# Kernel optimization log

Hardware: AMD Instinct MI355X
Metric: run time of the kernel (lower is better)

Reference implementation:

```python
import jax, jax.numpy as jnp
import numpy as np

NUM_PTS = 8   # num_points_per_face
K = 5         # self.k


def _sq_dist(x, y):
    # squared euclidean distance matrix (Nx, Ny); matches torch.cdist**2 / sum((a-b)**2)
    x2 = jnp.sum(x * x, axis=1)[:, None]
    y2 = jnp.sum(y * y, axis=1)[None, :]
    d = x2 + y2 - 2.0 * (x @ y.T)
    return jnp.maximum(d, 0.0)


def setup_inputs() -> dict:
    key = jax.random.key(0)
    k1, k2, k3, k4, k5, k6, k7 = jax.random.split(key, 7)
    V, Fs, Ft = 2048, 4096, 4096
    return {
        "source_vertices": jax.random.normal(k1, (1, V, 3), dtype=jnp.float32),
        "source_faces": jax.random.randint(k2, (Fs, 3), 0, V),
        "target_vertices": jax.random.normal(k3, (1, V, 3), dtype=jnp.float32),
        "target_faces": jax.random.randint(k4, (3, Ft), 0, V),
        "face_probs": jax.random.uniform(k5, (Fs,), dtype=jnp.float32),
        "r1u": jax.random.uniform(k6, (Fs, NUM_PTS), dtype=jnp.float32),
        "r2u": jax.random.uniform(k7, (Fs, NUM_PTS), dtype=jnp.float32),
    }


def reference(source_vertices, source_faces, target_vertices, target_faces, face_probs, r1u, r2u):
    sv = source_vertices[0]                 # (V, 3)
    tv = target_vertices[0]                 # (V, 3)
    tf = target_faces.T                     # (Ft, 3)
    Fs = source_faces.shape[0]

    src_bc = sv[source_faces].mean(axis=1)  # (Fs, 3) source barycenters
    tgt_bc = tv[tf].mean(axis=1)            # (Ft, 3) target barycenters

    # ---- forward loss: prob-weighted min squared distance to target barycenters
    d_fwd = _sq_dist(src_bc, tgt_bc)        # (Fs, Ft)
    forward_loss = jnp.sum(face_probs * jnp.min(d_fwd, axis=1))

    # ---- sample points from triangles via barycentric coords
    r1 = jnp.sqrt(r1u)
    w1 = 1.0 - r1
    w2 = r1 * (1.0 - r2u)
    w3 = r1 * r2u
    v1 = sv[source_faces[:, 0]]             # (Fs, 3)
    v2 = sv[source_faces[:, 1]]
    v3 = sv[source_faces[:, 2]]
    pts = (w1[..., None] * v1[:, None] + w2[..., None] * v2[:, None]
           + w3[..., None] * v3[:, None]).reshape(-1, 3)   # (P, 3), P = Fs*NUM_PTS
    pt_faces = jnp.repeat(jnp.arange(Fs), NUM_PTS)          # (P,)
    pt_probs = face_probs[pt_faces]                         # (P,)

    # ---- reverse loss, batched over all P points
    d_src = _sq_dist(pts, src_bc)                           # (P, Fs)
    neg_d, idx = jax.lax.top_k(-d_src, K + 1)               # K+1 smallest distances
    tri_dists = -neg_d                                      # (P, K+1)
    mask = idx != pt_faces[:, None]                         # exclude own face
    has_self = jnp.any(~mask, axis=1)
    excl_pos = jnp.where(has_self, jnp.argmin(mask, axis=1), K + 1)  # (P,)
    t = jnp.arange(K)
    sel = t[None, :] + (t[None, :] >= excl_pos[:, None]).astype(jnp.int32)  # (P, K)
    valid_dists = jnp.take_along_axis(tri_dists, sel, axis=1)   # (P, K)
    valid_idx = jnp.take_along_axis(idx, sel, axis=1)           # (P, K)
    valid_probs = face_probs[valid_idx]                         # (P, K)

    min_tgt = jnp.min(_sq_dist(pts, tgt_bc), axis=1)            # (P,)

    reverse_loss = jnp.sum(pt_probs * min_tgt
                           + (1.0 - pt_probs) * jnp.mean(valid_probs * valid_dists, axis=1))
    return forward_loss + reverse_loss
```

## Files before the change

kernel.cpp:

```cpp
#include <hip/hip_runtime.h>
#include <math.h>

#define FS 4096
#define FT 4096
#define TS 1024
#define BIGF 3.0e38f
#define KEYINF 0xFFFFFFFFu

__device__ __forceinline__ unsigned umin32(unsigned a, unsigned b) { return a < b ? a : b; }
__device__ __forceinline__ unsigned umax32(unsigned a, unsigned b) { return a < b ? b : a; }

__device__ __forceinline__ unsigned med3u(unsigned a, unsigned b, unsigned c) {
    unsigned d;
    asm("v_med3_u32 %0, %1, %2, %3" : "=v"(d) : "v"(a), "v"(b), "v"(c));
    return d;
}

__device__ __forceinline__ float block_reduce_sum(float v) {
    __shared__ float s[8];
    for (int o = 32; o > 0; o >>= 1) v += __shfl_down(v, o, 64);
    int lane = threadIdx.x & 63, wid = threadIdx.x >> 6;
    if (lane == 0) s[wid] = v;
    __syncthreads();
    int nw = blockDim.x >> 6;
    v = (threadIdx.x < (unsigned)nw) ? s[threadIdx.x] : 0.f;
    if (wid == 0)
        for (int o = 4; o > 0; o >>= 1) v += __shfl_down(v, o, 64);
    return v;
}

#define CE(x, y) { unsigned _n = umin32(x, y); y = umax32(x, y); x = _n; }

__device__ __forceinline__ void merge32(unsigned s[6]) {
    #pragma unroll
    for (int m = 1; m <= 16; m <<= 1) {
        unsigned b0 = __shfl_xor(s[0], m, 64), b1 = __shfl_xor(s[1], m, 64);
        unsigned b2 = __shfl_xor(s[2], m, 64), b3 = __shfl_xor(s[3], m, 64);
        unsigned b4 = __shfl_xor(s[4], m, 64), b5 = __shfl_xor(s[5], m, 64);
        unsigned l0 = s[0], l1 = s[1];
        unsigned l2 = umin32(s[2], b5), l3 = umin32(s[3], b4);
        unsigned l4 = umin32(s[4], b3), l5 = umin32(s[5], b2);
        unsigned l6 = b1, l7 = b0;
        CE(l0, l4) CE(l1, l5) CE(l2, l6) CE(l3, l7)
        CE(l0, l2) CE(l1, l3) CE(l4, l6) CE(l5, l7)
        CE(l0, l1) CE(l2, l3) CE(l4, l5) CE(l6, l7)
        s[0] = l0; s[1] = l1; s[2] = l2; s[3] = l3; s[4] = l4; s[5] = l5;
    }
}

__global__ __launch_bounds__(256) void k_prep(
        const float* __restrict__ sv, const int* __restrict__ sf,
        const float* __restrict__ tv, const int* __restrict__ tf,
        float4* __restrict__ sbc2, float4* __restrict__ tbc2,
        float4* __restrict__ sbcr, float* __restrict__ out) {
    int i = blockIdx.x * blockDim.x + threadIdx.x;
    if (i == 0) out[0] = 0.f;
    if (i >= FS) return;
    const float third = 1.f / 3.f;
    int a = sf[3*i], b = sf[3*i+1], c = sf[3*i+2];
    float x = (sv[3*a  ] + sv[3*b  ] + sv[3*c  ]) * third;
    float y = (sv[3*a+1] + sv[3*b+1] + sv[3*c+1]) * third;
    float z = (sv[3*a+2] + sv[3*b+2] + sv[3*c+2]) * third;
    float n2 = x*x + y*y + z*z;
    sbc2[i] = make_float4(-2.f*x, -2.f*y, -2.f*z, n2);
    sbcr[i] = make_float4(x, y, z, n2);
    int ta = tf[i], tb = tf[FT + i], tc = tf[2*FT + i];
    float tx = (tv[3*ta  ] + tv[3*tb  ] + tv[3*tc  ]) * third;
    float ty = (tv[3*ta+1] + tv[3*tb+1] + tv[3*tc+1]) * third;
    float tz = (tv[3*ta+2] + tv[3*tb+2] + tv[3*tc+2]) * third;
    tbc2[i] = make_float4(-2.f*tx, -2.f*ty, -2.f*tz, tx*tx + ty*ty + tz*tz);
}

__global__ __launch_bounds__(256, 4) void k_main(
        const float* __restrict__ sv, const int* __restrict__ sf,
        const float* __restrict__ fp,
        const float* __restrict__ r1u, const float* __restrict__ r2u,
        const float4* __restrict__ sbc2, const float4* __restrict__ tbc2,
        const float4* __restrict__ sbcr, float* __restrict__ out) {
    __shared__ float4 tileS[TS];
    __shared__ float4 tileT[TS];
    int tid  = threadIdx.x;
    int seg  = tid & 31;
    int slot = tid >> 5;
    float contrib = 0.f;

    if (blockIdx.x < 1024) {
        int pt0  = blockIdx.x * 32 + slot * 4;
        int face = pt0 >> 3;

        int a = sf[3*face], b = sf[3*face+1], c = sf[3*face+2];
        float ax = sv[3*a], ay = sv[3*a+1], az = sv[3*a+2];
        float bx = sv[3*b], by = sv[3*b+1], bz = sv[3*b+2];
        float cx = sv[3*c], cy = sv[3*c+1], cz = sv[3*c+2];
        float4 r14 = ((const float4*)r1u)[pt0 >> 2];
        float4 r24 = ((const float4*)r2u)[pt0 >> 2];
        float px[4], py[4], pz[4], p2[4];
        {
            float r1a[4] = {r14.x, r14.y, r14.z, r14.w};
            float r2a[4] = {r24.x, r24.y, r24.z, r24.w};
            #pragma unroll
            for (int i = 0; i < 4; ++i) {
                float r1 = sqrtf(r1a[i]);
                float w1 = 1.f - r1, w2 = r1 * (1.f - r2a[i]), w3 = r1 * r2a[i];
                px[i] = w1*ax + w2*bx + w3*cx;
                py[i] = w1*ay + w2*by + w3*cy;
                pz[i] = w1*az + w2*bz + w3*cz;
                p2[i] = px[i]*px[i] + py[i]*py[i] + pz[i]*pz[i];
            }
        }

        unsigned s0[4], s1[4], s2[4];
        #pragma unroll
        for (int i = 0; i < 4; ++i) { s0[i]=KEYINF; s1[i]=KEYINF; s2[i]=KEYINF; }
        float vm[4] = {BIGF, BIGF, BIGF, BIGF};

        for (int p = 0; p < 4; ++p) {
            int t0 = p * TS;
            #pragma unroll
            for (int j = 0; j < 4; ++j) {
                tileS[tid + j*256] = sbc2[t0 + tid + j*256];
                tileT[tid + j*256] = tbc2[t0 + tid + j*256];
            }
            __syncthreads();
            unsigned jj = (unsigned)(t0 + seg);
            #pragma unroll 4
            for (int jp = 0; jp < TS/32; ++jp) {
                float4 c4 = tileS[(jp << 5) + seg];
                #pragma unroll
                for (int i = 0; i < 4; ++i) {
                    float d = fmaf(px[i], c4.x, fmaf(py[i], c4.y,
                              fmaf(pz[i], c4.z, c4.w + p2[i])));
                    unsigned k = (__float_as_uint(d) & 0xFFFFF000u) | jj;
                    unsigned n0 = umin32(s0[i], k);
                    unsigned n1 = med3u(s0[i], s1[i], k);
                    unsigned n2 = med3u(s1[i], s2[i], k);
                    s0[i]=n0; s1[i]=n1; s2[i]=n2;
                }
                jj += 32;
            }
            #pragma unroll 4
            for (int jp = 0; jp < TS/32; ++jp) {
                float4 c4 = tileT[(jp << 5) + seg];
                #pragma unroll
                for (int i = 0; i < 4; ++i) {
                    float v = fmaf(px[i], c4.x, fmaf(py[i], c4.y, fmaf(pz[i], c4.z, c4.w)));
                    vm[i] = fminf(vm[i], v);
                }
            }
            __syncthreads();
        }

        #pragma unroll
        for (int i = 0; i < 4; ++i) {
            float v = vm[i];
            v = fminf(v, __shfl_xor(v, 1, 64));
            v = fminf(v, __shfl_xor(v, 2, 64));
            v = fminf(v, __shfl_xor(v, 4, 64));
            v = fminf(v, __shfl_xor(v, 8, 64));
            v = fminf(v, __shfl_xor(v, 16, 64));
            vm[i] = v;
        }

        float pf = fp[face];
        float csum = 0.f;
        #pragma unroll
        for (int i = 0; i < 4; ++i) {
            unsigned srt[6] = {s0[i], s1[i], s2[i], KEYINF, KEYINF, KEYINF};
            merge32(srt);
            if (seg == 0) {
                int   q0 = srt[0] & 0xFFF, q1 = srt[1] & 0xFFF, q2 = srt[2] & 0xFFF;
                int   q3 = srt[3] & 0xFFF, q4 = srt[4] & 0xFFF, q5 = srt[5] & 0xFFF;
                float d0 = __uint_as_float(srt[0] & 0xFFFFF000u);
                float d1 = __uint_as_float(srt[1] & 0xFFFFF000u);
                float d2 = __uint_as_float(srt[2] & 0xFFFFF000u);
                float d3 = __uint_as_float(srt[3] & 0xFFFFF000u);
                float d4 = __uint_as_float(srt[4] & 0xFFFFF000u);
                float d5 = __uint_as_float(srt[5] & 0xFFFFF000u);

                int skip = 5;
                if      (q0 == face) skip = 0;
                else if (q1 == face) skip = 1;
                else if (q2 == face) skip = 2;
                else if (q3 == face) skip = 3;
                else if (q4 == face) skip = 4;

                float s = 0.f;
                if (skip != 0) s += fp[q0] * d0;
                if (skip != 1) s += fp[q1] * d1;
                if (skip != 2) s += fp[q2] * d2;
                if (skip != 3) s += fp[q3] * d3;
                if (skip != 4) s += fp[q4] * d4;
                if (skip != 5) s += fp[q5] * d5;

                float mtd = fmaxf(vm[i] + p2[i], 0.f);
                csum += pf * mtd + (1.f - pf) * (s * 0.2f);
            }
        }
        if (seg == 0) contrib = csum;
    } else {
        int f0 = (blockIdx.x - 1024) * 32 + slot * 4;
        float4 q0 = sbcr[f0], q1 = sbcr[f0+1], q2 = sbcr[f0+2], q3 = sbcr[f0+3];
        float v0 = BIGF, v1 = BIGF, v2 = BIGF, v3 = BIGF;
        for (int p = 0; p < 4; ++p) {
            int t0 = p * TS;
            #pragma unroll
            for (int j = 0; j < 4; ++j) tileT[tid + j*256] = tbc2[t0 + tid + j*256];
            __syncthreads();
            #pragma unroll 4
            for (int jp = 0; jp < TS/32; ++jp) {
                float4 c4 = tileT[(jp << 5) + seg];
                v0 = fminf(v0, fmaf(q0.x, c4.x, fmaf(q0.y, c4.y, fmaf(q0.z, c4.z, c4.w))));
                v1 = fminf(v1, fmaf(q1.x, c4.x, fmaf(q1.y, c4.y, fmaf(q1.z, c4.z, c4.w))));
                v2 = fminf(v2, fmaf(q2.x, c4.x, fmaf(q2.y, c4.y, fmaf(q2.z, c4.z, c4.w))));
                v3 = fminf(v3, fmaf(q3.x, c4.x, fmaf(q3.y, c4.y, fmaf(q3.z, c4.z, c4.w))));
            }
            __syncthreads();
        }
        #pragma unroll
        for (int m = 1; m <= 16; m <<= 1) {
            v0 = fminf(v0, __shfl_xor(v0, m, 64));
            v1 = fminf(v1, __shfl_xor(v1, m, 64));
            v2 = fminf(v2, __shfl_xor(v2, m, 64));
            v3 = fminf(v3, __shfl_xor(v3, m, 64));
        }
        if (seg == 0)
            contrib = fp[f0  ] * fmaxf(v0 + q0.w, 0.f)
                    + fp[f0+1] * fmaxf(v1 + q1.w, 0.f)
                    + fp[f0+2] * fmaxf(v2 + q2.w, 0.f)
                    + fp[f0+3] * fmaxf(v3 + q3.w, 0.f);
    }

    float tot = block_reduce_sum(contrib);
    if (tid == 0) atomicAdd(out, tot);
}

extern "C" void kernel_launch(void* const* d_in, const int* in_sizes, int n_in,
                              void* d_out, int out_size, void* d_ws, size_t ws_size,
                              hipStream_t stream) {
    const float* sv  = (const float*)d_in[0];
    const int*   sf  = (const int*)  d_in[1];
    const float* tv  = (const float*)d_in[2];
    const int*   tf  = (const int*)  d_in[3];
    const float* fp  = (const float*)d_in[4];
    const float* r1u = (const float*)d_in[5];
    const float* r2u = (const float*)d_in[6];
    float* out = (float*)d_out;

    char* ws = (char*)d_ws;
    float4* sbc2 = (float4*)(ws);
    float4* tbc2 = (float4*)(ws + 65536);
    float4* sbcr = (float4*)(ws + 131072);

    k_prep<<<16,   256, 0, stream>>>(sv, sf, tv, tf, sbc2, tbc2, sbcr, out);
    k_main<<<1152, 256, 0, stream>>>(sv, sf, fp, r1u, r2u, sbc2, tbc2, sbcr, out);
}
```

Measured before the change: 118.9 us.

## Fold forward-loss min search into point blocks, drop separate forward blocks

The 128 extra blocks that computed the forward loss are removed. Each of the 1024 point blocks now also handles 4 source barycenters, reusing its already-loaded target tile: each warp half scans 16 of the 32 tile rows and the halves are merged through shared memory. The static shared array in the block reduction is replaced by a slice of the tile buffer, and the prep kernel is relaunched with 64-thread blocks. This removes a tail of extra blocks and duplicate target tile loads, but adds an extra barrier and some work per point block.

```diff
diff --git a/kernel.cpp b/kernel.cpp
--- a/kernel.cpp
+++ b/kernel.cpp
@@ -16,8 +16,7 @@
     return d;
 }
 
-__device__ __forceinline__ float block_reduce_sum(float v) {
-    __shared__ float s[8];
+__device__ __forceinline__ float block_reduce_sum(float v, float* s) {
     for (int o = 32; o > 0; o >>= 1) v += __shfl_down(v, o, 64);
     int lane = threadIdx.x & 63, wid = threadIdx.x >> 6;
     if (lane == 0) s[wid] = v;
@@ -48,12 +47,12 @@
     }
 }
 
-__global__ __launch_bounds__(256) void k_prep(
+__global__ __launch_bounds__(64) void k_prep(
         const float* __restrict__ sv, const int* __restrict__ sf,
         const float* __restrict__ tv, const int* __restrict__ tf,
         float4* __restrict__ sbc2, float4* __restrict__ tbc2,
         float4* __restrict__ sbcr, float* __restrict__ out) {
-    int i = blockIdx.x * blockDim.x + threadIdx.x;
+    int i = blockIdx.x * 64 + threadIdx.x;
     if (i == 0) out[0] = 0.f;
     if (i >= FS) return;
     const float third = 1.f / 3.f;
@@ -84,153 +83,147 @@
     int slot = tid >> 5;
     float contrib = 0.f;
 
-    if (blockIdx.x < 1024) {
-        int pt0  = blockIdx.x * 32 + slot * 4;
-        int face = pt0 >> 3;
-
-        int a = sf[3*face], b = sf[3*face+1], c = sf[3*face+2];
-        float ax = sv[3*a], ay = sv[3*a+1], az = sv[3*a+2];
-        float bx = sv[3*b], by = sv[3*b+1], bz = sv[3*b+2];
-        float cx = sv[3*c], cy = sv[3*c+1], cz = sv[3*c+2];
-        float4 r14 = ((const float4*)r1u)[pt0 >> 2];
-        float4 r24 = ((const float4*)r2u)[pt0 >> 2];
-        float px[4], py[4], pz[4], p2[4];
-        {
-            float r1a[4] = {r14.x, r14.y, r14.z, r14.w};
-            float r2a[4] = {r24.x, r24.y, r24.z, r24.w};
+    int pt0  = blockIdx.x * 32 + slot * 4;
+    int face = pt0 >> 3;
+
+    int a = sf[3*face], b = sf[3*face+1], c = sf[3*face+2];
+    float ax = sv[3*a], ay = sv[3*a+1], az = sv[3*a+2];
+    float bx = sv[3*b], by = sv[3*b+1], bz = sv[3*b+2];
+    float cx = sv[3*c], cy = sv[3*c+1], cz = sv[3*c+2];
+    float4 r14 = ((const float4*)r1u)[pt0 >> 2];
+    float4 r24 = ((const float4*)r2u)[pt0 >> 2];
+    float px[4], py[4], pz[4], p2[4];
+    {
+        float r1a[4] = {r14.x, r14.y, r14.z, r14.w};
+        float r2a[4] = {r24.x, r24.y, r24.z, r24.w};
+        #pragma unroll
+        for (int i = 0; i < 4; ++i) {
+            float r1 = sqrtf(r1a[i]);
+            float w1 = 1.f - r1, w2 = r1 * (1.f - r2a[i]), w3 = r1 * r2a[i];
+            px[i] = w1*ax + w2*bx + w3*cx;
+            py[i] = w1*ay + w2*by + w3*cy;
+            pz[i] = w1*az + w2*bz + w3*cz;
+            p2[i] = px[i]*px[i] + py[i]*py[i] + pz[i]*pz[i];
+        }
+    }
+
+    int fq = blockIdx.x * 4 + (slot & 3);
+    float4 qf = sbcr[fq];
+    float vfw = BIGF;
+    int jlo = (slot >> 2) << 4;
+
+    unsigned s0[4], s1[4], s2[4];
+    #pragma unroll
+    for (int i = 0; i < 4; ++i) { s0[i]=KEYINF; s1[i]=KEYINF; s2[i]=KEYINF; }
+    float vm[4] = {BIGF, BIGF, BIGF, BIGF};
+
+    for (int p = 0; p < 4; ++p) {
+        int t0 = p * TS;
+        #pragma unroll
+        for (int j = 0; j < 4; ++j) {
+            tileS[tid + j*256] = sbc2[t0 + tid + j*256];
+            tileT[tid + j*256] = tbc2[t0 + tid + j*256];
+        }
+        __syncthreads();
+        unsigned jj = (unsigned)(t0 + seg);
+        #pragma unroll 4
+        for (int jp = 0; jp < TS/32; ++jp) {
+            float4 c4 = tileS[(jp << 5) + seg];
             #pragma unroll
             for (int i = 0; i < 4; ++i) {
-                float r1 = sqrtf(r1a[i]);
-                float w1 = 1.f - r1, w2 = r1 * (1.f - r2a[i]), w3 = r1 * r2a[i];
-                px[i] = w1*ax + w2*bx + w3*cx;
-                py[i] = w1*ay + w2*by + w3*cy;
-                pz[i] = w1*az + w2*bz + w3*cz;
-                p2[i] = px[i]*px[i] + py[i]*py[i] + pz[i]*pz[i];
+                float d = fmaf(px[i], c4.x, fmaf(py[i], c4.y,
+                          fmaf(pz[i], c4.z, c4.w + p2[i])));
+                unsigned k = (__float_as_uint(d) & 0xFFFFF000u) | jj;
+                unsigned n0 = umin32(s0[i], k);
+                unsigned n1 = med3u(s0[i], s1[i], k);
+                unsigned n2 = med3u(s1[i], s2[i], k);
+                s0[i]=n0; s1[i]=n1; s2[i]=n2;
             }
-        }
-
-        unsigned s0[4], s1[4], s2[4];
-        #pragma unroll
-        for (int i = 0; i < 4; ++i) { s0[i]=KEYINF; s1[i]=KEYINF; s2[i]=KEYINF; }
-        float vm[4] = {BIGF, BIGF, BIGF, BIGF};
-
-        for (int p = 0; p < 4; ++p) {
-            int t0 = p * TS;
+            jj += 32;
+        }
+        #pragma unroll 4
+        for (int jp = 0; jp < TS/32; ++jp) {
+            float4 c4 = tileT[(jp << 5) + seg];
             #pragma unroll
-            for (int j = 0; j < 4; ++j) {
-                tileS[tid + j*256] = sbc2[t0 + tid + j*256];
-                tileT[tid + j*256] = tbc2[t0 + tid + j*256];
+            for (int i = 0; i < 4; ++i) {
+                float v = fmaf(px[i], c4.x, fmaf(py[i], c4.y, fmaf(pz[i], c4.z, c4.w)));
+                vm[i] = fminf(vm[i], v);
             }
-            __syncthreads();
-            unsigned jj = (unsigned)(t0 + seg);
-            #pragma unroll 4
-            for (int jp = 0; jp < TS/32; ++jp) {
-                float4 c4 = tileS[(jp << 5) + seg];
-                #pragma unroll
-                for (int i = 0; i < 4; ++i) {
-                    float d = fmaf(px[i], c4.x, fmaf(py[i], c4.y,
-                              fmaf(pz[i], c4.z, c4.w + p2[i])));
-                    unsigned k = (__float_as_uint(d) & 0xFFFFF000u) | jj;
-                    unsigned n0 = umin32(s0[i], k);
-                    unsigned n1 = med3u(s0[i], s1[i], k);
-                    unsigned n2 = med3u(s1[i], s2[i], k);
-                    s0[i]=n0; s1[i]=n1; s2[i]=n2;
-                }
-                jj += 32;
-            }
-            #pragma unroll 4
-            for (int jp = 0; jp < TS/32; ++jp) {
-                float4 c4 = tileT[(jp << 5) + seg];
-                #pragma unroll
-                for (int i = 0; i < 4; ++i) {
-                    float v = fmaf(px[i], c4.x, fmaf(py[i], c4.y, fmaf(pz[i], c4.z, c4.w)));
-                    vm[i] = fminf(vm[i], v);
-                }
-            }
-            __syncthreads();
-        }
-
-        #pragma unroll
-        for (int i = 0; i < 4; ++i) {
-            float v = vm[i];
-            v = fminf(v, __shfl_xor(v, 1, 64));
-            v = fminf(v, __shfl_xor(v, 2, 64));
-            v = fminf(v, __shfl_xor(v, 4, 64));
-            v = fminf(v, __shfl_xor(v, 8, 64));
-            v = fminf(v, __shfl_xor(v, 16, 64));
-            vm[i] = v;
-        }
-
-        float pf = fp[face];
-        float csum = 0.f;
-        #pragma unroll
-        for (int i = 0; i < 4; ++i) {
-            unsigned srt[6] = {s0[i], s1[i], s2[i], KEYINF, KEYINF, KEYINF};
-            merge32(srt);
-            if (seg == 0) {
-                int   q0 = srt[0] & 0xFFF, q1 = srt[1] & 0xFFF, q2 = srt[2] & 0xFFF;
-                int   q3 = srt[3] & 0xFFF, q4 = srt[4] & 0xFFF, q5 = srt[5] & 0xFFF;
-                float d0 = __uint_as_float(srt[0] & 0xFFFFF000u);
-                float d1 = __uint_as_float(srt[1] & 0xFFFFF000u);
-                float d2 = __uint_as_float(srt[2] & 0xFFFFF000u);
-                float d3 = __uint_as_float(srt[3] & 0xFFFFF000u);
-                float d4 = __uint_as_float(srt[4] & 0xFFFFF000u);
-                float d5 = __uint_as_float(srt[5] & 0xFFFFF000u);
-
-                int skip = 5;
-                if      (q0 == face) skip = 0;
-                else if (q1 == face) skip = 1;
-                else if (q2 == face) skip = 2;
-                else if (q3 == face) skip = 3;
-                else if (q4 == face) skip = 4;
-
-                float s = 0.f;
-                if (skip != 0) s += fp[q0] * d0;
-                if (skip != 1) s += fp[q1] * d1;
-                if (skip != 2) s += fp[q2] * d2;
-                if (skip != 3) s += fp[q3] * d3;
-                if (skip != 4) s += fp[q4] * d4;
-                if (skip != 5) s += fp[q5] * d5;
-
-                float mtd = fmaxf(vm[i] + p2[i], 0.f);
-                csum += pf * mtd + (1.f - pf) * (s * 0.2f);
-            }
-        }
-        if (seg == 0) contrib = csum;
-    } else {
-        int f0 = (blockIdx.x - 1024) * 32 + slot * 4;
-        float4 q0 = sbcr[f0], q1 = sbcr[f0+1], q2 = sbcr[f0+2], q3 = sbcr[f0+3];
-        float v0 = BIGF, v1 = BIGF, v2 = BIGF, v3 = BIGF;
-        for (int p = 0; p < 4; ++p) {
-            int t0 = p * TS;
-            #pragma unroll
-            for (int j = 0; j < 4; ++j) tileT[tid + j*256] = tbc2[t0 + tid + j*256];
-            __syncthreads();
-            #pragma unroll 4
-            for (int jp = 0; jp < TS/32; ++jp) {
-                float4 c4 = tileT[(jp << 5) + seg];
-                v0 = fminf(v0, fmaf(q0.x, c4.x, fmaf(q0.y, c4.y, fmaf(q0.z, c4.z, c4.w))));
-                v1 = fminf(v1, fmaf(q1.x, c4.x, fmaf(q1.y, c4.y, fmaf(q1.z, c4.z, c4.w))));
-                v2 = fminf(v2, fmaf(q2.x, c4.x, fmaf(q2.y, c4.y, fmaf(q2.z, c4.z, c4.w))));
-                v3 = fminf(v3, fmaf(q3.x, c4.x, fmaf(q3.y, c4.y, fmaf(q3.z, c4.z, c4.w))));
-            }
-            __syncthreads();
-        }
-        #pragma unroll
-        for (int m = 1; m <= 16; m <<= 1) {
-            v0 = fminf(v0, __shfl_xor(v0, m, 64));
-            v1 = fminf(v1, __shfl_xor(v1, m, 64));
-            v2 = fminf(v2, __shfl_xor(v2, m, 64));
-            v3 = fminf(v3, __shfl_xor(v3, m, 64));
-        }
-        if (seg == 0)
-            contrib = fp[f0  ] * fmaxf(v0 + q0.w, 0.f)
-                    + fp[f0+1] * fmaxf(v1 + q1.w, 0.f)
-                    + fp[f0+2] * fmaxf(v2 + q2.w, 0.f)
-                    + fp[f0+3] * fmaxf(v3 + q3.w, 0.f);
-    }
-
-    float tot = block_reduce_sum(contrib);
+        }
+        #pragma unroll 4
+        for (int jq = 0; jq < 16; ++jq) {
+            float4 c4 = tileT[((jlo + jq) << 5) + seg];
+            vfw = fminf(vfw, fmaf(qf.x, c4.x, fmaf(qf.y, c4.y, fmaf(qf.z, c4.z, c4.w))));
+        }
+        __syncthreads();
+    }
+
+    #pragma unroll
+    for (int i = 0; i < 4; ++i) {
+        float v = vm[i];
+        v = fminf(v, __shfl_xor(v, 1, 64));
+        v = fminf(v, __shfl_xor(v, 2, 64));
+        v = fminf(v, __shfl_xor(v, 4, 64));
+        v = fminf(v, __shfl_xor(v, 8, 64));
+        v = fminf(v, __shfl_xor(v, 16, 64));
+        vm[i] = v;
+    }
+
+    {
+        float v = vfw;
+        v = fminf(v, __shfl_xor(v, 1, 64));
+        v = fminf(v, __shfl_xor(v, 2, 64));
+        v = fminf(v, __shfl_xor(v, 4, 64));
+        v = fminf(v, __shfl_xor(v, 8, 64));
+        v = fminf(v, __shfl_xor(v, 16, 64));
+        vfw = v;
+    }
+    float* fwdS = (float*)tileS;
+    if (seg == 0 && slot >= 4) fwdS[slot] = vfw;
+    __syncthreads();
+    if (seg == 0 && slot < 4) {
+        float v2 = fminf(vfw, fwdS[slot + 4]);
+        contrib += fp[fq] * fmaxf(v2 + qf.w, 0.f);
+    }
+
+    float pf = fp[face];
+    float csum = 0.f;
+    #pragma unroll
+    for (int i = 0; i < 4; ++i) {
+        unsigned srt[6] = {s0[i], s1[i], s2[i], KEYINF, KEYINF, KEYINF};
+        merge32(srt);
+        if (seg == 0) {
+            int   q0 = srt[0] & 0xFFF, q1 = srt[1] & 0xFFF, q2 = srt[2] & 0xFFF;
+            int   q3 = srt[3] & 0xFFF, q4 = srt[4] & 0xFFF, q5 = srt[5] & 0xFFF;
+            float d0 = __uint_as_float(srt[0] & 0xFFFFF000u);
+            float d1 = __uint_as_float(srt[1] & 0xFFFFF000u);
+            float d2 = __uint_as_float(srt[2] & 0xFFFFF000u);
+            float d3 = __uint_as_float(srt[3] & 0xFFFFF000u);
+            float d4 = __uint_as_float(srt[4] & 0xFFFFF000u);
+            float d5 = __uint_as_float(srt[5] & 0xFFFFF000u);
+
+            int skip = 5;
+            if      (q0 == face) skip = 0;
+            else if (q1 == face) skip = 1;
+            else if (q2 == face) skip = 2;
+            else if (q3 == face) skip = 3;
+            else if (q4 == face) skip = 4;
+
+            float s = 0.f;
+            if (skip != 0) s += fp[q0] * d0;
+            if (skip != 1) s += fp[q1] * d1;
+            if (skip != 2) s += fp[q2] * d2;
+            if (skip != 3) s += fp[q3] * d3;
+            if (skip != 4) s += fp[q4] * d4;
+            if (skip != 5) s += fp[q5] * d5;
+
+            float mtd = fmaxf(vm[i] + p2[i], 0.f);
+            csum += pf * mtd + (1.f - pf) * (s * 0.2f);
+        }
+    }
+    if (seg == 0) contrib += csum;
+
+    float tot = block_reduce_sum(contrib, (float*)tileS + 8);
     if (tid == 0) atomicAdd(out, tot);
 }
 
@@ -251,6 +244,6 @@
     float4* tbc2 = (float4*)(ws + 65536);
     float4* sbcr = (float4*)(ws + 131072);
 
-    k_prep<<<16,   256, 0, stream>>>(sv, sf, tv, tf, sbc2, tbc2, sbcr, out);
-    k_main<<<1152, 256, 0, stream>>>(sv, sf, fp, r1u, r2u, sbc2, tbc2, sbcr, out);
-}
+    k_prep<<<64,   64,  0, stream>>>(sv, sf, tv, tf, sbc2, tbc2, sbcr, out);
+    k_main<<<1024, 256, 0, stream>>>(sv, sf, fp, r1u, r2u, sbc2, tbc2, sbcr, out);
+}
```

Measured after the change: 124.7 us. +4.9%, slower.

## Interleave barycenter tiles in pairs and use packed FP32 FMA for distances

Applied to the files above, without the earlier changes.

The prep kernel now writes source and target barycenter coefficients in a pair-interleaved layout, so each float4 holds the x,y (or z,w) components of two candidates 32 apart. The main loops load two float4s per step and evaluate two candidates at once with v_pk_fma_f32/v_pk_add_f32, roughly halving the scalar FMA instruction count for the distance computations. The top-3 insertion and the min updates remain scalar per candidate. The point coordinates are broadcast into packed registers, which raises register pressure, and the prep launch shape changes to 64 threads per block.

```diff
diff --git a/kernel.cpp b/kernel.cpp
--- a/kernel.cpp
+++ b/kernel.cpp
@@ -7,12 +7,25 @@
 #define BIGF 3.0e38f
 #define KEYINF 0xFFFFFFFFu
 
+typedef float v2f __attribute__((ext_vector_type(2)));
+
 __device__ __forceinline__ unsigned umin32(unsigned a, unsigned b) { return a < b ? a : b; }
 __device__ __forceinline__ unsigned umax32(unsigned a, unsigned b) { return a < b ? b : a; }
 
 __device__ __forceinline__ unsigned med3u(unsigned a, unsigned b, unsigned c) {
     unsigned d;
     asm("v_med3_u32 %0, %1, %2, %3" : "=v"(d) : "v"(a), "v"(b), "v"(c));
+    return d;
+}
+
+__device__ __forceinline__ v2f pk_fma(v2f a, v2f b, v2f c) {
+    v2f d;
+    asm("v_pk_fma_f32 %0, %1, %2, %3" : "=v"(d) : "v"(a), "v"(b), "v"(c));
+    return d;
+}
+__device__ __forceinline__ v2f pk_add(v2f a, v2f b) {
+    v2f d;
+    asm("v_pk_add_f32 %0, %1, %2" : "=v"(d) : "v"(a), "v"(b));
     return d;
 }
 
@@ -48,12 +61,12 @@
     }
 }
 
-__global__ __launch_bounds__(256) void k_prep(
+__global__ __launch_bounds__(64) void k_prep(
         const float* __restrict__ sv, const int* __restrict__ sf,
         const float* __restrict__ tv, const int* __restrict__ tf,
         float4* __restrict__ sbc2, float4* __restrict__ tbc2,
         float4* __restrict__ sbcr, float* __restrict__ out) {
-    int i = blockIdx.x * blockDim.x + threadIdx.x;
+    int i = blockIdx.x * 64 + threadIdx.x;
     if (i == 0) out[0] = 0.f;
     if (i >= FS) return;
     const float third = 1.f / 3.f;
@@ -62,13 +75,22 @@
     float y = (sv[3*a+1] + sv[3*b+1] + sv[3*c+1]) * third;
     float z = (sv[3*a+2] + sv[3*b+2] + sv[3*c+2]) * third;
     float n2 = x*x + y*y + z*z;
-    sbc2[i] = make_float4(-2.f*x, -2.f*y, -2.f*z, n2);
     sbcr[i] = make_float4(x, y, z, n2);
     int ta = tf[i], tb = tf[FT + i], tc = tf[2*FT + i];
     float tx = (tv[3*ta  ] + tv[3*tb  ] + tv[3*tc  ]) * third;
     float ty = (tv[3*ta+1] + tv[3*tb+1] + tv[3*tc+1]) * third;
     float tz = (tv[3*ta+2] + tv[3*tb+2] + tv[3*tc+2]) * third;
-    tbc2[i] = make_float4(-2.f*tx, -2.f*ty, -2.f*tz, tx*tx + ty*ty + tz*tz);
+    float tn2 = tx*tx + ty*ty + tz*tz;
+
+    int tt = i >> 10, cc = i & 1023;
+    int g = cc >> 6, half = (cc >> 5) & 1, pp = cc & 31;
+    int lo4 = tt*1024 + g*32 + pp, hi4 = lo4 + 512;
+    float* S = (float*)sbc2;
+    S[4*lo4 + half]     = -2.f*x;  S[4*lo4 + 2 + half] = -2.f*y;
+    S[4*hi4 + half]     = -2.f*z;  S[4*hi4 + 2 + half] = n2;
+    float* T = (float*)tbc2;
+    T[4*lo4 + half]     = -2.f*tx; T[4*lo4 + 2 + half] = -2.f*ty;
+    T[4*hi4 + half]     = -2.f*tz; T[4*hi4 + 2 + half] = tn2;
 }
 
 __global__ __launch_bounds__(256, 4) void k_main(
@@ -94,7 +116,8 @@
         float cx = sv[3*c], cy = sv[3*c+1], cz = sv[3*c+2];
         float4 r14 = ((const float4*)r1u)[pt0 >> 2];
         float4 r24 = ((const float4*)r2u)[pt0 >> 2];
-        float px[4], py[4], pz[4], p2[4];
+        float p2s[4];
+        v2f pxb[4], pyb[4], pzb[4], p2b[4];
         {
             float r1a[4] = {r14.x, r14.y, r14.z, r14.w};
             float r2a[4] = {r24.x, r24.y, r24.z, r24.w};
@@ -102,17 +125,22 @@
             for (int i = 0; i < 4; ++i) {
                 float r1 = sqrtf(r1a[i]);
                 float w1 = 1.f - r1, w2 = r1 * (1.f - r2a[i]), w3 = r1 * r2a[i];
-                px[i] = w1*ax + w2*bx + w3*cx;
-                py[i] = w1*ay + w2*by + w3*cy;
-                pz[i] = w1*az + w2*bz + w3*cz;
-                p2[i] = px[i]*px[i] + py[i]*py[i] + pz[i]*pz[i];
+                float px = w1*ax + w2*bx + w3*cx;
+                float py = w1*ay + w2*by + w3*cy;
+                float pz = w1*az + w2*bz + w3*cz;
+                float p2 = px*px + py*py + pz*pz;
+                p2s[i] = p2;
+                pxb[i] = (v2f){px, px}; pyb[i] = (v2f){py, py};
+                pzb[i] = (v2f){pz, pz}; p2b[i] = (v2f){p2, p2};
             }
         }
 
         unsigned s0[4], s1[4], s2[4];
         #pragma unroll
         for (int i = 0; i < 4; ++i) { s0[i]=KEYINF; s1[i]=KEYINF; s2[i]=KEYINF; }
-        float vm[4] = {BIGF, BIGF, BIGF, BIGF};
+        v2f vm2[4];
+        #pragma unroll
+        for (int i = 0; i < 4; ++i) vm2[i] = (v2f){BIGF, BIGF};
 
         for (int p = 0; p < 4; ++p) {
             int t0 = p * TS;
@@ -122,37 +150,54 @@
                 tileT[tid + j*256] = tbc2[t0 + tid + j*256];
             }
             __syncthreads();
-            unsigned jj = (unsigned)(t0 + seg);
+            unsigned jja = (unsigned)(t0 + seg);
             #pragma unroll 4
-            for (int jp = 0; jp < TS/32; ++jp) {
-                float4 c4 = tileS[(jp << 5) + seg];
+            for (int jp = 0; jp < 16; ++jp) {
+                float4 lo = tileS[(jp << 5) + seg];
+                float4 hi = tileS[512 + (jp << 5) + seg];
+                v2f cx2 = {lo.x, lo.y}, cy2 = {lo.z, lo.w};
+                v2f cz2 = {hi.x, hi.y}, cw2 = {hi.z, hi.w};
                 #pragma unroll
                 for (int i = 0; i < 4; ++i) {
-                    float d = fmaf(px[i], c4.x, fmaf(py[i], c4.y,
-                              fmaf(pz[i], c4.z, c4.w + p2[i])));
-                    unsigned k = (__float_as_uint(d) & 0xFFFFF000u) | jj;
-                    unsigned n0 = umin32(s0[i], k);
-                    unsigned n1 = med3u(s0[i], s1[i], k);
-                    unsigned n2 = med3u(s1[i], s2[i], k);
+                    v2f d2 = pk_add(cw2, p2b[i]);
+                    d2 = pk_fma(pzb[i], cz2, d2);
+                    d2 = pk_fma(pyb[i], cy2, d2);
+                    d2 = pk_fma(pxb[i], cx2, d2);
+                    unsigned ka = (__float_as_uint(d2.x) & 0xFFFFF000u) | jja;
+                    unsigned kb = (__float_as_uint(d2.y) & 0xFFFFF000u) | (jja + 32u);
+                    unsigned n0 = umin32(s0[i], ka);
+                    unsigned n1 = med3u(s0[i], s1[i], ka);
+                    unsigned n2 = med3u(s1[i], s2[i], ka);
+                    s0[i]=n0; s1[i]=n1; s2[i]=n2;
+                    n0 = umin32(s0[i], kb);
+                    n1 = med3u(s0[i], s1[i], kb);
+                    n2 = med3u(s1[i], s2[i], kb);
                     s0[i]=n0; s1[i]=n1; s2[i]=n2;
                 }
-                jj += 32;
+                jja += 64;
             }
             #pragma unroll 4
-            for (int jp = 0; jp < TS/32; ++jp) {
-                float4 c4 = tileT[(jp << 5) + seg];
+            for (int jp = 0; jp < 16; ++jp) {
+                float4 lo = tileT[(jp << 5) + seg];
+                float4 hi = tileT[512 + (jp << 5) + seg];
+                v2f cx2 = {lo.x, lo.y}, cy2 = {lo.z, lo.w};
+                v2f cz2 = {hi.x, hi.y}, cw2 = {hi.z, hi.w};
                 #pragma unroll
                 for (int i = 0; i < 4; ++i) {
-                    float v = fmaf(px[i], c4.x, fmaf(py[i], c4.y, fmaf(pz[i], c4.z, c4.w)));
-                    vm[i] = fminf(vm[i], v);
+                    v2f t = pk_fma(pzb[i], cz2, cw2);
+                    t = pk_fma(pyb[i], cy2, t);
+                    t = pk_fma(pxb[i], cx2, t);
+                    vm2[i].x = fminf(vm2[i].x, t.x);
+                    vm2[i].y = fminf(vm2[i].y, t.y);
                 }
             }
             __syncthreads();
         }
 
+        float vm[4];
         #pragma unroll
         for (int i = 0; i < 4; ++i) {
-            float v = vm[i];
+            float v = fminf(vm2[i].x, vm2[i].y);
             v = fminf(v, __shfl_xor(v, 1, 64));
             v = fminf(v, __shfl_xor(v, 2, 64));
             v = fminf(v, __shfl_xor(v, 4, 64));
@@ -192,42 +237,63 @@
                 if (skip != 4) s += fp[q4] * d4;
                 if (skip != 5) s += fp[q5] * d5;
 
-                float mtd = fmaxf(vm[i] + p2[i], 0.f);
+                float mtd = fmaxf(vm[i] + p2s[i], 0.f);
                 csum += pf * mtd + (1.f - pf) * (s * 0.2f);
             }
         }
         if (seg == 0) contrib = csum;
     } else {
         int f0 = (blockIdx.x - 1024) * 32 + slot * 4;
-        float4 q0 = sbcr[f0], q1 = sbcr[f0+1], q2 = sbcr[f0+2], q3 = sbcr[f0+3];
-        float v0 = BIGF, v1 = BIGF, v2 = BIGF, v3 = BIGF;
+        float qw[4];
+        v2f qxb[4], qyb[4], qzb[4];
+        #pragma unroll
+        for (int i = 0; i < 4; ++i) {
+            float4 q = sbcr[f0 + i];
+            qxb[i] = (v2f){q.x, q.x}; qyb[i] = (v2f){q.y, q.y};
+            qzb[i] = (v2f){q.z, q.z}; qw[i] = q.w;
+        }
+        v2f vf2[4];
+        #pragma unroll
+        for (int i = 0; i < 4; ++i) vf2[i] = (v2f){BIGF, BIGF};
+
         for (int p = 0; p < 4; ++p) {
             int t0 = p * TS;
             #pragma unroll
             for (int j = 0; j < 4; ++j) tileT[tid + j*256] = tbc2[t0 + tid + j*256];
             __syncthreads();
             #pragma unroll 4
-            for (int jp = 0; jp < TS/32; ++jp) {
-                float4 c4 = tileT[(jp << 5) + seg];
-                v0 = fminf(v0, fmaf(q0.x, c4.x, fmaf(q0.y, c4.y, fmaf(q0.z, c4.z, c4.w))));
-                v1 = fminf(v1, fmaf(q1.x, c4.x, fmaf(q1.y, c4.y, fmaf(q1.z, c4.z, c4.w))));
-                v2 = fminf(v2, fmaf(q2.x, c4.x, fmaf(q2.y, c4.y, fmaf(q2.z, c4.z, c4.w))));
-                v3 = fminf(v3, fmaf(q3.x, c4.x, fmaf(q3.y, c4.y, fmaf(q3.z, c4.z, c4.w))));
+            for (int jp = 0; jp < 16; ++jp) {
+                float4 lo = tileT[(jp << 5) + seg];
+                float4 hi = tileT[512 + (jp << 5) + seg];
+                v2f cx2 = {lo.x, lo.y}, cy2 = {lo.z, lo.w};
+                v2f cz2 = {hi.x, hi.y}, cw2 = {hi.z, hi.w};
+                #pragma unroll
+                for (int i = 0; i < 4; ++i) {
+                    v2f t = pk_fma(qzb[i], cz2, cw2);
+                    t = pk_fma(qyb[i], cy2, t);
+                    t = pk_fma(qxb[i], cx2, t);
+                    vf2[i].x = fminf(vf2[i].x, t.x);
+                    vf2[i].y = fminf(vf2[i].y, t.y);
+                }
             }
             __syncthreads();
         }
-        #pragma unroll
-        for (int m = 1; m <= 16; m <<= 1) {
-            v0 = fminf(v0, __shfl_xor(v0, m, 64));
-            v1 = fminf(v1, __shfl_xor(v1, m, 64));
-            v2 = fminf(v2, __shfl_xor(v2, m, 64));
-            v3 = fminf(v3, __shfl_xor(v3, m, 64));
+        float vf[4];
+        #pragma unroll
+        for (int i = 0; i < 4; ++i) {
+            float v = fminf(vf2[i].x, vf2[i].y);
+            v = fminf(v, __shfl_xor(v, 1, 64));
+            v = fminf(v, __shfl_xor(v, 2, 64));
+            v = fminf(v, __shfl_xor(v, 4, 64));
+            v = fminf(v, __shfl_xor(v, 8, 64));
+            v = fminf(v, __shfl_xor(v, 16, 64));
+            vf[i] = v;
         }
         if (seg == 0)
-            contrib = fp[f0  ] * fmaxf(v0 + q0.w, 0.f)
-                    + fp[f0+1] * fmaxf(v1 + q1.w, 0.f)
-                    + fp[f0+2] * fmaxf(v2 + q2.w, 0.f)
-                    + fp[f0+3] * fmaxf(v3 + q3.w, 0.f);
+            contrib = fp[f0  ] * fmaxf(vf[0] + qw[0], 0.f)
+                    + fp[f0+1] * fmaxf(vf[1] + qw[1], 0.f)
+                    + fp[f0+2] * fmaxf(vf[2] + qw[2], 0.f)
+                    + fp[f0+3] * fmaxf(vf[3] + qw[3], 0.f);
     }
 
     float tot = block_reduce_sum(contrib);
@@ -251,6 +317,6 @@
     float4* tbc2 = (float4*)(ws + 65536);
     float4* sbcr = (float4*)(ws + 131072);
 
-    k_prep<<<16,   256, 0, stream>>>(sv, sf, tv, tf, sbc2, tbc2, sbcr, out);
+    k_prep<<<64,   64,  0, stream>>>(sv, sf, tv, tf, sbc2, tbc2, sbcr, out);
     k_main<<<1152, 256, 0, stream>>>(sv, sf, fp, r1u, r2u, sbc2, tbc2, sbcr, out);
 }
```

Result: faster. 114.4 us (-3.8%).
